# Optimization experiments

Hardware: AMD Instinct MI355X
Metric: run time of the kernel (lower is better)

## Reference

```python
import jax, jax.numpy as jnp
import numpy as np
from jax import lax


def avg_pool3(x):
    # F.avg_pool2d(x, 3, 1, 1) with count_include_pad=True: zero-pad, divide by 9.
    s = lax.reduce_window(x, 0.0, lax.add, (1, 1, 3, 3), (1, 1, 1, 1),
                          [(0, 0), (0, 0), (1, 1), (1, 1)])
    return s / 9.0


def resize_bilinear_ac(x, H, W):
    # bilinear resize with align_corners=True, separable gathers
    B, C, h, w = x.shape
    if (h, w) == (H, W):
        return x
    yc = jnp.linspace(0.0, h - 1.0, H)
    xc = jnp.linspace(0.0, w - 1.0, W)
    y0 = jnp.floor(yc).astype(jnp.int32); y1 = jnp.minimum(y0 + 1, h - 1)
    x0 = jnp.floor(xc).astype(jnp.int32); x1 = jnp.minimum(x0 + 1, w - 1)
    wy = (yc - y0).astype(x.dtype)
    wx = (xc - x0).astype(x.dtype)
    xr = x[:, :, y0, :] * (1.0 - wy)[None, None, :, None] + x[:, :, y1, :] * wy[None, None, :, None]
    return xr[:, :, :, x0] * (1.0 - wx) + xr[:, :, :, x1] * wx


def grid_sample_border(img, grid):
    # F.grid_sample(mode='bilinear', padding_mode='border', align_corners=True)
    B, C, H, W = img.shape
    x = jnp.clip((grid[..., 0] + 1.0) * 0.5 * (W - 1), 0.0, W - 1.0)
    y = jnp.clip((grid[..., 1] + 1.0) * 0.5 * (H - 1), 0.0, H - 1.0)
    x0 = jnp.floor(x).astype(jnp.int32); y0 = jnp.floor(y).astype(jnp.int32)
    x1 = jnp.minimum(x0 + 1, W - 1); y1 = jnp.minimum(y0 + 1, H - 1)
    wx = (x - x0)[..., None]; wy = (y - y0)[..., None]
    imt = jnp.transpose(img, (0, 2, 3, 1))  # [B,H,W,C]
    b = jnp.arange(B)[:, None, None]
    v00 = imt[b, y0, x0]; v01 = imt[b, y0, x1]
    v10 = imt[b, y1, x0]; v11 = imt[b, y1, x1]
    top = v00 * (1.0 - wx) + v01 * wx
    bot = v10 * (1.0 - wx) + v11 * wx
    out = top * (1.0 - wy) + bot * wy
    return jnp.transpose(out, (0, 3, 1, 2))


def warp_image(img, flow):
    B, C, H, W = img.shape
    _, _, h, w = flow.shape
    flow = resize_bilinear_ac(flow, H, W)
    scale = jnp.array([W / w, H / h], dtype=img.dtype).reshape(1, 2, 1, 1)
    flow = flow * scale
    yy, xx = jnp.meshgrid(jnp.linspace(-1.0, 1.0, H, dtype=img.dtype),
                          jnp.linspace(-1.0, 1.0, W, dtype=img.dtype), indexing='ij')
    base = jnp.stack((xx, yy), axis=-1)[None]  # [1,H,W,2]
    fn = jnp.stack([2.0 * flow[:, 0] / max(W - 1, 1),
                    2.0 * flow[:, 1] / max(H - 1, 1)], axis=-1)  # [B,H,W,2]
    return grid_sample_border(img, base + fn)


def ssim_map(x, y, C1=0.01 ** 2, C2=0.03 ** 2):
    mu_x = avg_pool3(x); mu_y = avg_pool3(y)
    sigma_x = avg_pool3(x * x) - mu_x * mu_x
    sigma_y = avg_pool3(y * y) - mu_y * mu_y
    sigma_xy = avg_pool3(x * y) - mu_x * mu_y
    ssim = (2 * mu_x * mu_y + C1) * (2 * sigma_xy + C2) / \
           ((mu_x ** 2 + mu_y ** 2 + C1) * (sigma_x + sigma_y + C2) + 1e-12)
    return jnp.mean(jnp.clip((1.0 - ssim) / 2.0, 0.0, 1.0), axis=1, keepdims=True)


def masked_mean(x, mask):
    m = (mask > 0.5).astype(x.dtype)
    num = jnp.sum(x * m)
    den = jnp.maximum(jnp.sum(m), 1.0)
    return num / den


def smoothness_loss(flow):
    dx = jnp.abs(flow[:, :, :, :-1] - flow[:, :, :, 1:])
    dy = jnp.abs(flow[:, :, :-1, :] - flow[:, :, 1:, :])
    return jnp.mean(dx) + jnp.mean(dy)


def setup_inputs() -> dict:
    key = jax.random.key(0)
    k1, k2, k3, k4 = jax.random.split(key, 4)
    B, H, W = 8, 512, 1024
    h, w = 128, 256
    return {
        'flow': jax.random.normal(k1, (B, 2, h, w), dtype=jnp.float32),
        'img1': jax.random.uniform(k2, (B, 3, H, W), dtype=jnp.float32),
        'img2': jax.random.uniform(k3, (B, 3, H, W), dtype=jnp.float32),
        'valid_mask': jax.random.uniform(k4, (B, 1, H, W), dtype=jnp.float32),
    }


def reference(flow, img1, img2, valid_mask):
    alpha_photo, alpha_smooth = 1.0, 0.1
    img2_warp = warp_image(img2, flow)
    l1 = jnp.mean(jnp.abs(img1 - img2_warp), axis=1, keepdims=True)
    photo_map = 0.85 * ssim_map(img1, img2_warp) + 0.15 * l1
    photo = masked_mean(photo_map, valid_mask)
    smooth = smoothness_loss(flow)
    total = alpha_photo * photo + alpha_smooth * smooth
    return (total, photo, smooth)
```

## Files before the change

### kernel.cpp

```cpp
#include <hip/hip_runtime.h>

#define B_   8
#define H_   512
#define W_   1024
#define FH_  128
#define FW_  256
#define TW   32
#define TH   8
#define NSLOT 256

__device__ __forceinline__ float wave_reduce(float v) {
    #pragma unroll
    for (int off = 32; off > 0; off >>= 1) v += __shfl_down(v, off, 64);
    return v;
}

__global__ __launch_bounds__(256)
void fused_main(const float* __restrict__ flow, const float* __restrict__ img1,
                const float* __restrict__ img2, const float* __restrict__ mask,
                float* __restrict__ accum) {
    const int b   = blockIdx.z;
    const int tx0 = blockIdx.x * TW;
    const int ty0 = blockIdx.y * TH;
    const int tid = threadIdx.x;

    __shared__ float s1[3][TH + 2][TW + 4];
    __shared__ float s2[3][TH + 2][TW + 4];

    const size_t plane = (size_t)H_ * W_;
    const float* f0  = flow + (size_t)b * 2 * FH_ * FW_;
    const float* f1  = f0 + FH_ * FW_;
    const float* i1b = img1 + (size_t)b * 3 * plane;
    const float* i2b = img2 + (size_t)b * 3 * plane;

    for (int i = tid; i < (TH + 2) * (TW + 2); i += 256) {
        const int ly = i / (TW + 2);
        const int lx = i - ly * (TW + 2);
        const int gy = ty0 + ly - 1;
        const int gx = tx0 + lx - 1;
        float v1[3] = {0.f, 0.f, 0.f};
        float v2[3] = {0.f, 0.f, 0.f};
        if (gy >= 0 && gy < H_ && gx >= 0 && gx < W_) {
            const size_t p = (size_t)gy * W_ + gx;
            v1[0] = i1b[p];
            v1[1] = i1b[p + plane];
            v1[2] = i1b[p + 2 * plane];

            const float yc = gy * (127.0f / 511.0f);
            const float xc = gx * (255.0f / 1023.0f);
            const int y0 = (int)yc, x0 = (int)xc;
            const int y1 = min(y0 + 1, FH_ - 1);
            const int x1 = min(x0 + 1, FW_ - 1);
            const float wy = yc - y0, wx = xc - x0;
            const int r0 = y0 * FW_, r1 = y1 * FW_;
            const float fx = (f0[r0 + x0] * (1.f - wx) + f0[r0 + x1] * wx) * (1.f - wy)
                           + (f0[r1 + x0] * (1.f - wx) + f0[r1 + x1] * wx) * wy;
            const float fy = (f1[r0 + x0] * (1.f - wx) + f1[r0 + x1] * wx) * (1.f - wy)
                           + (f1[r1 + x0] * (1.f - wx) + f1[r1 + x1] * wx) * wy;

            const float gxs = fminf(fmaxf((float)gx + 4.0f * fx, 0.0f), (float)(W_ - 1));
            const float gys = fminf(fmaxf((float)gy + 4.0f * fy, 0.0f), (float)(H_ - 1));
            const int sx0 = (int)gxs, sy0 = (int)gys;
            const int sx1 = min(sx0 + 1, W_ - 1);
            const int sy1 = min(sy0 + 1, H_ - 1);
            const float swx = gxs - sx0, swy = gys - sy0;
            const size_t p00 = (size_t)sy0 * W_ + sx0;
            const size_t p01 = (size_t)sy0 * W_ + sx1;
            const size_t p10 = (size_t)sy1 * W_ + sx0;
            const size_t p11 = (size_t)sy1 * W_ + sx1;
            #pragma unroll
            for (int c = 0; c < 3; ++c) {
                const float* im = i2b + (size_t)c * plane;
                const float top = im[p00] * (1.f - swx) + im[p01] * swx;
                const float bot = im[p10] * (1.f - swx) + im[p11] * swx;
                v2[c] = top * (1.f - swy) + bot * swy;
            }
        }
        #pragma unroll
        for (int c = 0; c < 3; ++c) { s1[c][ly][lx] = v1[c]; s2[c][ly][lx] = v2[c]; }
    }
    __syncthreads();

    const int lx = tid & (TW - 1);
    const int ly = tid >> 5;
    const int gx = tx0 + lx;
    const int gy = ty0 + ly;

    const float inv9 = 1.0f / 9.0f;
    const float C1 = 0.0001f, C2 = 0.0009f;
    float distSum = 0.f, l1sum = 0.f;
    #pragma unroll
    for (int c = 0; c < 3; ++c) {
        float sx = 0.f, sy = 0.f, sxx = 0.f, syy = 0.f, sxy = 0.f;
        #pragma unroll
        for (int dy = 0; dy < 3; ++dy) {
            #pragma unroll
            for (int dx = 0; dx < 3; ++dx) {
                const float a = s1[c][ly + dy][lx + dx];
                const float b2 = s2[c][ly + dy][lx + dx];
                sx += a; sy += b2;
                sxx = fmaf(a, a, sxx);
                syy = fmaf(b2, b2, syy);
                sxy = fmaf(a, b2, sxy);
            }
        }
        const float mx = sx * inv9, my = sy * inv9;
        const float vx = sxx * inv9 - mx * mx;
        const float vy = syy * inv9 - my * my;
        const float vxy = sxy * inv9 - mx * my;
        const float ssim = (2.f * mx * my + C1) * (2.f * vxy + C2) /
                           ((mx * mx + my * my + C1) * (vx + vy + C2) + 1e-12f);
        distSum += fminf(fmaxf((1.0f - ssim) * 0.5f, 0.f), 1.f);
        l1sum += fabsf(s1[c][ly + 1][lx + 1] - s2[c][ly + 1][lx + 1]);
    }
    const float pm = 0.85f * (distSum * (1.0f / 3.0f)) + 0.15f * (l1sum * (1.0f / 3.0f));
    const float m  = (mask[(size_t)b * plane + (size_t)gy * W_ + gx] > 0.5f) ? 1.f : 0.f;

    float num = wave_reduce(pm * m);
    float den = wave_reduce(m);
    __shared__ float rn[4], rd[4];
    const int wid = tid >> 6, lane = tid & 63;
    if (lane == 0) { rn[wid] = num; rd[wid] = den; }
    __syncthreads();
    if (tid == 0) {
        const int lin  = (blockIdx.z * gridDim.y + blockIdx.y) * gridDim.x + blockIdx.x;
        float* slot = accum + (size_t)(lin & (NSLOT - 1)) * 4;
        atomicAdd(&slot[0], rn[0] + rn[1] + rn[2] + rn[3]);
        atomicAdd(&slot[1], rd[0] + rd[1] + rd[2] + rd[3]);
    }
}

__global__ __launch_bounds__(256)
void smooth_kernel(const float* __restrict__ flow, float* __restrict__ accum) {
    const int N = B_ * 2 * FH_ * FW_;
    float dxs = 0.f, dys = 0.f;
    for (int i = blockIdx.x * 256 + threadIdx.x; i < N; i += gridDim.x * 256) {
        const float f = flow[i];
        const int x = i & (FW_ - 1);
        const int y = (i >> 8) & (FH_ - 1);
        if (x < FW_ - 1) dxs += fabsf(f - flow[i + 1]);
        if (y < FH_ - 1) dys += fabsf(f - flow[i + FW_]);
    }
    dxs = wave_reduce(dxs);
    dys = wave_reduce(dys);
    __shared__ float rn[4], rd[4];
    const int wid = threadIdx.x >> 6, lane = threadIdx.x & 63;
    if (lane == 0) { rn[wid] = dxs; rd[wid] = dys; }
    __syncthreads();
    if (threadIdx.x == 0) {
        float* slot = accum + (size_t)blockIdx.x * 4;
        atomicAdd(&slot[2], rn[0] + rn[1] + rn[2] + rn[3]);
        atomicAdd(&slot[3], rd[0] + rd[1] + rd[2] + rd[3]);
    }
}

__global__ __launch_bounds__(256)
void finalize_kernel(const float* __restrict__ accum, float* __restrict__ out) {
    const int t = threadIdx.x;
    float num = accum[t * 4 + 0];
    float den = accum[t * 4 + 1];
    float dxs = accum[t * 4 + 2];
    float dys = accum[t * 4 + 3];
    num = wave_reduce(num); den = wave_reduce(den);
    dxs = wave_reduce(dxs); dys = wave_reduce(dys);
    __shared__ float r[4][4];
    const int wid = t >> 6, lane = t & 63;
    if (lane == 0) { r[wid][0] = num; r[wid][1] = den; r[wid][2] = dxs; r[wid][3] = dys; }
    __syncthreads();
    if (t == 0) {
        const float tn = r[0][0] + r[1][0] + r[2][0] + r[3][0];
        const float td = r[0][1] + r[1][1] + r[2][1] + r[3][1];
        const float tx = r[0][2] + r[1][2] + r[2][2] + r[3][2];
        const float ty = r[0][3] + r[1][3] + r[2][3] + r[3][3];
        const float photo   = tn / fmaxf(td, 1.0f);
        const float mean_dx = tx / (float)(B_ * 2 * FH_ * (FW_ - 1));
        const float mean_dy = ty / (float)(B_ * 2 * (FH_ - 1) * FW_);
        const float smooth  = mean_dx + mean_dy;
        out[0] = photo + 0.1f * smooth;
        out[1] = photo;
        out[2] = smooth;
    }
}

extern "C" void kernel_launch(void* const* d_in, const int* in_sizes, int n_in,
                              void* d_out, int out_size, void* d_ws, size_t ws_size,
                              hipStream_t stream) {
    const float* flow = (const float*)d_in[0];
    const float* img1 = (const float*)d_in[1];
    const float* img2 = (const float*)d_in[2];
    const float* mask = (const float*)d_in[3];
    float* out   = (float*)d_out;
    float* accum = (float*)d_ws;

    hipMemsetAsync(accum, 0, NSLOT * 4 * sizeof(float), stream);
    smooth_kernel<<<NSLOT, 256, 0, stream>>>(flow, accum);
    dim3 grid(W_ / TW, H_ / TH, B_);
    fused_main<<<grid, 256, 0, stream>>>(flow, img1, img2, mask, accum);
    finalize_kernel<<<1, 256, 0, stream>>>(accum, out);
}
```

Measured before the change: 214.6 us.

## Enlarge tile and compute four rows per thread with sliding-window SSIM sums

```diff
diff --git a/kernel.cpp b/kernel.cpp
--- a/kernel.cpp
+++ b/kernel.cpp
@@ -5,14 +5,27 @@
 #define W_   1024
 #define FH_  128
 #define FW_  256
-#define TW   32
-#define TH   8
+#define TW   64
+#define TH   16
+#define HW_  (TW + 2)
+#define HH_  (TH + 2)
 #define NSLOT 256
 
 __device__ __forceinline__ float wave_reduce(float v) {
     #pragma unroll
     for (int off = 32; off > 0; off >>= 1) v += __shfl_down(v, off, 64);
     return v;
+}
+
+__device__ __forceinline__ void hrow(const float* __restrict__ a, const float* __restrict__ b,
+                                     float& hA, float& hB, float& hAA, float& hBB, float& hAB) {
+    const float a0 = a[0], a1 = a[1], a2 = a[2];
+    const float b0 = b[0], b1 = b[1], b2 = b[2];
+    hA  = a0 + a1 + a2;
+    hB  = b0 + b1 + b2;
+    hAA = fmaf(a0, a0, fmaf(a1, a1, a2 * a2));
+    hBB = fmaf(b0, b0, fmaf(b1, b1, b2 * b2));
+    hAB = fmaf(a0, b0, fmaf(a1, b1, a2 * b2));
 }
 
 __global__ __launch_bounds__(256)
@@ -24,106 +37,144 @@
     const int ty0 = blockIdx.y * TH;
     const int tid = threadIdx.x;
 
-    __shared__ float s1[3][TH + 2][TW + 4];
-    __shared__ float s2[3][TH + 2][TW + 4];
-
-    const size_t plane = (size_t)H_ * W_;
+    __shared__ float s1[3][HH_][HW_];
+    __shared__ float s2[3][HH_][HW_];
+
+    const uint32_t plane = (uint32_t)H_ * W_;
     const float* f0  = flow + (size_t)b * 2 * FH_ * FW_;
     const float* f1  = f0 + FH_ * FW_;
-    const float* i1b = img1 + (size_t)b * 3 * plane;
-    const float* i2b = img2 + (size_t)b * 3 * plane;
-
-    for (int i = tid; i < (TH + 2) * (TW + 2); i += 256) {
-        const int ly = i / (TW + 2);
-        const int lx = i - ly * (TW + 2);
+    const float* i10 = img1 + (size_t)b * 3 * plane;
+    const float* i11 = i10 + plane;
+    const float* i12 = i11 + plane;
+    const float* i20 = img2 + (size_t)b * 3 * plane;
+    const float* i21 = i20 + plane;
+    const float* i22 = i21 + plane;
+
+    for (int i = tid; i < HH_ * HW_; i += 256) {
+        const int ly = i / HW_;
+        const int lx = i - ly * HW_;
         const int gy = ty0 + ly - 1;
         const int gx = tx0 + lx - 1;
-        float v1[3] = {0.f, 0.f, 0.f};
-        float v2[3] = {0.f, 0.f, 0.f};
+        float v10 = 0.f, v11 = 0.f, v12 = 0.f;
+        float v20 = 0.f, v21 = 0.f, v22 = 0.f;
         if (gy >= 0 && gy < H_ && gx >= 0 && gx < W_) {
-            const size_t p = (size_t)gy * W_ + gx;
-            v1[0] = i1b[p];
-            v1[1] = i1b[p + plane];
-            v1[2] = i1b[p + 2 * plane];
+            const uint32_t p = (uint32_t)gy * W_ + (uint32_t)gx;
+            v10 = i10[p]; v11 = i11[p]; v12 = i12[p];
 
             const float yc = gy * (127.0f / 511.0f);
             const float xc = gx * (255.0f / 1023.0f);
             const int y0 = (int)yc, x0 = (int)xc;
-            const int y1 = min(y0 + 1, FH_ - 1);
-            const int x1 = min(x0 + 1, FW_ - 1);
-            const float wy = yc - y0, wx = xc - x0;
-            const int r0 = y0 * FW_, r1 = y1 * FW_;
-            const float fx = (f0[r0 + x0] * (1.f - wx) + f0[r0 + x1] * wx) * (1.f - wy)
-                           + (f0[r1 + x0] * (1.f - wx) + f0[r1 + x1] * wx) * wy;
-            const float fy = (f1[r0 + x0] * (1.f - wx) + f1[r0 + x1] * wx) * (1.f - wy)
-                           + (f1[r1 + x0] * (1.f - wx) + f1[r1 + x1] * wx) * wy;
-
-            const float gxs = fminf(fmaxf((float)gx + 4.0f * fx, 0.0f), (float)(W_ - 1));
-            const float gys = fminf(fmaxf((float)gy + 4.0f * fy, 0.0f), (float)(H_ - 1));
+            const int y1i = min(y0 + 1, FH_ - 1);
+            const int x1i = min(x0 + 1, FW_ - 1);
+            const float wy = yc - (float)y0, wx = xc - (float)x0;
+            const uint32_t r0 = (uint32_t)y0 * FW_;
+            const uint32_t r1 = (uint32_t)y1i * FW_;
+            const float a00 = f0[r0 + x0], a01 = f0[r0 + x1i];
+            const float a10 = f0[r1 + x0], a11 = f0[r1 + x1i];
+            const float c00 = f1[r0 + x0], c01 = f1[r0 + x1i];
+            const float c10 = f1[r1 + x0], c11 = f1[r1 + x1i];
+            const float fxt = a00 + wx * (a01 - a00);
+            const float fxb = a10 + wx * (a11 - a10);
+            const float fx  = fxt + wy * (fxb - fxt);
+            const float fyt = c00 + wx * (c01 - c00);
+            const float fyb = c10 + wx * (c11 - c10);
+            const float fy  = fyt + wy * (fyb - fyt);
+
+            const float gxs = fminf(fmaxf(fmaf(4.0f, fx, (float)gx), 0.0f), (float)(W_ - 1));
+            const float gys = fminf(fmaxf(fmaf(4.0f, fy, (float)gy), 0.0f), (float)(H_ - 1));
             const int sx0 = (int)gxs, sy0 = (int)gys;
             const int sx1 = min(sx0 + 1, W_ - 1);
             const int sy1 = min(sy0 + 1, H_ - 1);
-            const float swx = gxs - sx0, swy = gys - sy0;
-            const size_t p00 = (size_t)sy0 * W_ + sx0;
-            const size_t p01 = (size_t)sy0 * W_ + sx1;
-            const size_t p10 = (size_t)sy1 * W_ + sx0;
-            const size_t p11 = (size_t)sy1 * W_ + sx1;
-            #pragma unroll
-            for (int c = 0; c < 3; ++c) {
-                const float* im = i2b + (size_t)c * plane;
-                const float top = im[p00] * (1.f - swx) + im[p01] * swx;
-                const float bot = im[p10] * (1.f - swx) + im[p11] * swx;
-                v2[c] = top * (1.f - swy) + bot * swy;
+            const float swx = gxs - (float)sx0, swy = gys - (float)sy0;
+            const uint32_t p00 = (uint32_t)sy0 * W_ + (uint32_t)sx0;
+            const uint32_t p01 = (uint32_t)sy0 * W_ + (uint32_t)sx1;
+            const uint32_t p10 = (uint32_t)sy1 * W_ + (uint32_t)sx0;
+            const uint32_t p11 = (uint32_t)sy1 * W_ + (uint32_t)sx1;
+
+            {
+                const float t = i20[p00] + swx * (i20[p01] - i20[p00]);
+                const float u = i20[p10] + swx * (i20[p11] - i20[p10]);
+                v20 = t + swy * (u - t);
+            }
+            {
+                const float t = i21[p00] + swx * (i21[p01] - i21[p00]);
+                const float u = i21[p10] + swx * (i21[p11] - i21[p10]);
+                v21 = t + swy * (u - t);
+            }
+            {
+                const float t = i22[p00] + swx * (i22[p01] - i22[p00]);
+                const float u = i22[p10] + swx * (i22[p11] - i22[p10]);
+                v22 = t + swy * (u - t);
             }
         }
-        #pragma unroll
-        for (int c = 0; c < 3; ++c) { s1[c][ly][lx] = v1[c]; s2[c][ly][lx] = v2[c]; }
-    }
-    __syncthreads();
-
-    const int lx = tid & (TW - 1);
-    const int ly = tid >> 5;
-    const int gx = tx0 + lx;
-    const int gy = ty0 + ly;
+        s1[0][ly][lx] = v10; s1[1][ly][lx] = v11; s1[2][ly][lx] = v12;
+        s2[0][ly][lx] = v20; s2[1][ly][lx] = v21; s2[2][ly][lx] = v22;
+    }
+
+    const int lx  = tid & 63;
+    const int lyg = tid >> 6;
+    const int rb  = lyg * 4;
+    const float* mb = mask + (size_t)b * plane;
+    const uint32_t mb0 = (uint32_t)(ty0 + rb) * W_ + (uint32_t)(tx0 + lx);
+    float mreg[4];
+    #pragma unroll
+    for (int k = 0; k < 4; ++k) mreg[k] = mb[mb0 + (uint32_t)k * W_];
+
+    __syncthreads();
 
     const float inv9 = 1.0f / 9.0f;
     const float C1 = 0.0001f, C2 = 0.0009f;
-    float distSum = 0.f, l1sum = 0.f;
+    float dist[4] = {0.f, 0.f, 0.f, 0.f};
+    float l1s [4] = {0.f, 0.f, 0.f, 0.f};
+
     #pragma unroll
     for (int c = 0; c < 3; ++c) {
-        float sx = 0.f, sy = 0.f, sxx = 0.f, syy = 0.f, sxy = 0.f;
+        float hA0,hB0,hAA0,hBB0,hAB0;
+        float hA1,hB1,hAA1,hBB1,hAB1;
+        float hA2,hB2,hAA2,hBB2,hAB2;
+        hrow(&s1[c][rb + 0][lx], &s2[c][rb + 0][lx], hA0,hB0,hAA0,hBB0,hAB0);
+        hrow(&s1[c][rb + 1][lx], &s2[c][rb + 1][lx], hA1,hB1,hAA1,hBB1,hAB1);
         #pragma unroll
-        for (int dy = 0; dy < 3; ++dy) {
-            #pragma unroll
-            for (int dx = 0; dx < 3; ++dx) {
-                const float a = s1[c][ly + dy][lx + dx];
-                const float b2 = s2[c][ly + dy][lx + dx];
-                sx += a; sy += b2;
-                sxx = fmaf(a, a, sxx);
-                syy = fmaf(b2, b2, syy);
-                sxy = fmaf(a, b2, sxy);
-            }
+        for (int k = 0; k < 4; ++k) {
+            hrow(&s1[c][rb + k + 2][lx], &s2[c][rb + k + 2][lx], hA2,hB2,hAA2,hBB2,hAB2);
+            const float sA  = hA0  + hA1  + hA2;
+            const float sB  = hB0  + hB1  + hB2;
+            const float sAA = hAA0 + hAA1 + hAA2;
+            const float sBB = hBB0 + hBB1 + hBB2;
+            const float sAB = hAB0 + hAB1 + hAB2;
+            const float mx  = sA * inv9, my = sB * inv9;
+            const float vx  = fmaf(-mx, mx, sAA * inv9);
+            const float vy  = fmaf(-my, my, sBB * inv9);
+            const float vxy = fmaf(-mx, my, sAB * inv9);
+            const float numt = (2.f * mx * my + C1) * (2.f * vxy + C2);
+            const float dent = fmaf(fmaf(mx, mx, fmaf(my, my, C1)), (vx + vy + C2), 1e-12f);
+            const float ssim = numt * __builtin_amdgcn_rcpf(dent);
+            dist[k] += fminf(fmaxf((1.0f - ssim) * 0.5f, 0.f), 1.f);
+            const float ac = s1[c][rb + k + 1][lx + 1];
+            const float bc = s2[c][rb + k + 1][lx + 1];
+            l1s[k] += fabsf(ac - bc);
+            hA0 = hA1; hB0 = hB1; hAA0 = hAA1; hBB0 = hBB1; hAB0 = hAB1;
+            hA1 = hA2; hB1 = hB2; hAA1 = hAA2; hBB1 = hBB2; hAB1 = hAB2;
         }
-        const float mx = sx * inv9, my = sy * inv9;
-        const float vx = sxx * inv9 - mx * mx;
-        const float vy = syy * inv9 - my * my;
-        const float vxy = sxy * inv9 - mx * my;
-        const float ssim = (2.f * mx * my + C1) * (2.f * vxy + C2) /
-                           ((mx * mx + my * my + C1) * (vx + vy + C2) + 1e-12f);
-        distSum += fminf(fmaxf((1.0f - ssim) * 0.5f, 0.f), 1.f);
-        l1sum += fabsf(s1[c][ly + 1][lx + 1] - s2[c][ly + 1][lx + 1]);
-    }
-    const float pm = 0.85f * (distSum * (1.0f / 3.0f)) + 0.15f * (l1sum * (1.0f / 3.0f));
-    const float m  = (mask[(size_t)b * plane + (size_t)gy * W_ + gx] > 0.5f) ? 1.f : 0.f;
-
-    float num = wave_reduce(pm * m);
-    float den = wave_reduce(m);
+    }
+
+    float num_acc = 0.f, den_acc = 0.f;
+    #pragma unroll
+    for (int k = 0; k < 4; ++k) {
+        const float pmv = 0.28333334f * dist[k] + 0.05f * l1s[k];
+        const float m   = (mreg[k] > 0.5f) ? 1.f : 0.f;
+        num_acc = fmaf(pmv, m, num_acc);
+        den_acc += m;
+    }
+
+    float num = wave_reduce(num_acc);
+    float den = wave_reduce(den_acc);
     __shared__ float rn[4], rd[4];
     const int wid = tid >> 6, lane = tid & 63;
     if (lane == 0) { rn[wid] = num; rd[wid] = den; }
     __syncthreads();
     if (tid == 0) {
-        const int lin  = (blockIdx.z * gridDim.y + blockIdx.y) * gridDim.x + blockIdx.x;
+        const int lin = (blockIdx.z * gridDim.y + blockIdx.y) * gridDim.x + blockIdx.x;
         float* slot = accum + (size_t)(lin & (NSLOT - 1)) * 4;
         atomicAdd(&slot[0], rn[0] + rn[1] + rn[2] + rn[3]);
         atomicAdd(&slot[1], rd[0] + rd[1] + rd[2] + rd[3]);
```

After: 204.7 us. 1.05x faster.
